# Performance work log

Hardware: AMD Instinct MI355X
Metric: run time of the kernel (lower is better)

The kernel has to match this reference:

```python
import jax, jax.numpy as jnp
import numpy as np

B, T, D = 8, 2048, 1024
DK, DV = 1024, 1024


def setup_inputs() -> dict:
    key = jax.random.key(0)
    ks = jax.random.split(key, 11)
    s = 0.02
    return {
        "query": jax.random.normal(ks[0], (B, T, D), jnp.float32),
        "keys": jax.random.normal(ks[1], (B, T, D), jnp.float32),
        "values": jax.random.normal(ks[2], (B, T, D), jnp.float32),
        "Wq": jax.random.normal(ks[3], (D, DK), jnp.float32) * s,
        "bq": jnp.zeros((DK,), jnp.float32),
        "Wk": jax.random.normal(ks[4], (D, DK), jnp.float32) * s,
        "bk": jnp.zeros((DK,), jnp.float32),
        "Wv": jax.random.normal(ks[5], (D, DV), jnp.float32) * s,
        "bv": jnp.zeros((DV,), jnp.float32),
        "Wo": jax.random.normal(ks[6], (DV, D), jnp.float32) * s,
        "bo": jnp.zeros((D,), jnp.float32),
        "apply_mask": 1,
    }


def reference(query, keys, values, Wq, bq, Wk, bk, Wv, bv, Wo, bo, apply_mask):
    # input projections
    q = query @ Wq + bq   # [B, T, DK]
    k = keys @ Wk + bk    # [B, T, DK]
    v = values @ Wv + bv  # [B, T, DV]
    dk = jnp.asarray(DK, jnp.float32)
    # explicit full score matrix, as in the original (non-flash) module
    scores = jnp.einsum("btd,bsd->bts", q, k) / jnp.sqrt(dk)  # [B, T, T]
    if apply_mask:
        Tq = q.shape[1]
        causal = jnp.triu(jnp.ones((Tq, Tq), bool), 1)  # True above diagonal
        scores = jnp.where(causal[None, :, :], -jnp.inf, scores)
    weights = jax.nn.softmax(scores, axis=-1)
    context = jnp.einsum("bts,bsd->btd", weights, v)  # [B, T, DV]
    return context @ Wo + bo  # [B, T, D]
```

## Files before the change

### kernel.cpp

```cpp
#include <hip/hip_runtime.h>
#include <hip/hip_bf16.h>


typedef __attribute__((ext_vector_type(8))) short bf16x8;
typedef __attribute__((ext_vector_type(4))) float f32x4;

#define DEVI __device__ __forceinline__
#define VM_GATE(n) asm volatile("s_waitcnt vmcnt(" #n ")" ::: "memory")
#define LGKM0()    asm volatile("s_waitcnt lgkmcnt(0)" ::: "memory")

DEVI unsigned short f2bf(float f) {
  union { float f; unsigned u; } v; v.f = f;
  unsigned r = v.u + 0x7FFFu + ((v.u >> 16) & 1u);
  return (unsigned short)(r >> 16);
}

DEVI unsigned pkbf(float a, float b) {
  unsigned r;
  asm("v_cvt_pk_bf16_f32 %0, %1, %2" : "=v"(r) : "v"(a), "v"(b));
  return r;
}

DEVI void load_lds16(const void* g, void* l) {
  __builtin_amdgcn_global_load_lds(
      (const __attribute__((address_space(1))) unsigned int*)g,
      (__attribute__((address_space(3))) unsigned int*)l,
      16, 0, 0);
}

constexpr int BM = 256, BN = 256, BK = 64;

DEVI void stage_chunk(char* chunk, const unsigned short* src, long ldx,
                      int kbase, int tid) {
#pragma unroll
  for (int i = 0; i < 2; ++i) {
    int tloc = i * 512 + tid;
    int r = tloc >> 2, ps = tloc & 3;
    int q = (ps - (r >> 1)) & 3;
    load_lds16(src + (size_t)r * ldx + kbase + q * 8,
               chunk + (i * 512 + (tid & 0x1C0)) * 16);
  }
}

DEVI bf16x8 frag(const char* chunk, int r, int q0) {
  int sp = (q0 + (r >> 1)) & 3;
  return *(const bf16x8*)(chunk + r * 64 + sp * 16);
}

DEVI void a32_load(float4* fr, const float* src, long lda, int kbase, int tid) {
#pragma unroll
  for (int j = 0; j < 4; ++j) {
    int cell = j * 512 + tid;
    int r = cell >> 3, q = cell & 7;
    const float* p = src + (size_t)r * lda + kbase + q * 8;
    fr[2 * j]     = *(const float4*)p;
    fr[2 * j + 1] = *(const float4*)(p + 4);
  }
}
DEVI void a32_write(char* chunk0, char* chunk1, const float4* fr, int tid) {
#pragma unroll
  for (int j = 0; j < 4; ++j) {
    int cell = j * 512 + tid;
    int r = cell >> 3, q = cell & 7;
    int kh = q >> 2, qq = q & 3;
    int sp = (qq + (r >> 1)) & 3;
    uint4 u;
    u.x = pkbf(fr[2 * j].x,     fr[2 * j].y);
    u.y = pkbf(fr[2 * j].z,     fr[2 * j].w);
    u.z = pkbf(fr[2 * j + 1].x, fr[2 * j + 1].y);
    u.w = pkbf(fr[2 * j + 1].z, fr[2 * j + 1].w);
    *(uint4*)((kh ? chunk1 : chunk0) + r * 64 + sp * 16) = u;
  }
}

template<bool A_F32, bool OUT_F32, bool OUT_TRANS, bool DO_BIAS, bool DO_SCALE,
         bool DO_CSKIP, bool DO_KCLAMP>
__global__ __launch_bounds__(512, 2) void gemm_k(
    const void* __restrict__ Ap, long lda, long sAz,
    const unsigned short* __restrict__ Bt, long ldb, long sBz,
    void* __restrict__ Cp, long ldc, long sCz,
    const float* __restrict__ bias, float scale,
    const int* __restrict__ maskp, int Kdim)
{
  const int nx = gridDim.x, ny = gridDim.y;
  int bid = (blockIdx.z * ny + blockIdx.y) * nx + blockIdx.x;
  const int nwg = nx * ny * (int)gridDim.z;
  if ((nwg & 7) == 0) bid = (bid & 7) * (nwg >> 3) + (bid >> 3);
  const int bx = bid % nx;
  const int t1 = bid / nx;
  const int by = t1 % ny;
  const int z  = t1 / ny;

  const int n0 = bx * BN;
  const int m0 = by * BM;
  if constexpr (DO_CSKIP) {
    if (maskp[0] && n0 > m0 + (BM - 1)) return;
  }
  int Keff = Kdim;
  if constexpr (DO_KCLAMP) {
    if (maskp[0]) Keff = min(Kdim, m0 + BM);
  }

  __shared__ alignas(16) char LDSb[2][2][2][16384];

  const int tid  = threadIdx.x;
  const int lane = tid & 63;
  const int w    = tid >> 6;
  const int wr   = w >> 2, wc = w & 3;
  const int la   = lane & 15;
  const int q0   = lane >> 4;

  f32x4 acc[8][4];
  const f32x4 z4 = {0.f, 0.f, 0.f, 0.f};
#pragma unroll
  for (int mi = 0; mi < 8; ++mi)
#pragma unroll
    for (int ni = 0; ni < 4; ++ni) acc[mi][ni] = z4;

  const unsigned short* Ag0 = (const unsigned short*)Ap + (size_t)z * sAz + (size_t)m0 * lda;
  const float*          Af0 = (const float*)Ap + (size_t)z * sAz + (size_t)m0 * lda;
  const unsigned short* Bg0 = Bt + (size_t)z * sBz + (size_t)n0 * ldb;

  float4 fr[8];

  if constexpr (A_F32) {
    a32_load(fr, Af0, lda, 0, tid);
    stage_chunk((char*)LDSb[0][1][0], Bg0, ldb, 0,  tid);
    stage_chunk((char*)LDSb[0][1][1], Bg0, ldb, 32, tid);
    VM_GATE(4);
    a32_write((char*)LDSb[0][0][0], (char*)LDSb[0][0][1], fr, tid);
    LGKM0();
  } else {
    stage_chunk((char*)LDSb[0][0][0], Ag0, lda, 0,  tid);
    stage_chunk((char*)LDSb[0][1][0], Bg0, ldb, 0,  tid);
    stage_chunk((char*)LDSb[0][0][1], Ag0, lda, 32, tid);
    stage_chunk((char*)LDSb[0][1][1], Bg0, ldb, 32, tid);
  }

  const int nt = Keff / BK;
  for (int t = 0; t < nt; ++t) {
    const int buf = t & 1, nb = buf ^ 1;
    const bool pf = (t + 1 < nt);
    const int kb = (t + 1) * BK;
    const char* Ak0 = LDSb[buf][0][0];
    const char* Bk0 = LDSb[buf][1][0];
    const char* Ak1 = LDSb[buf][0][1];
    const char* Bk1 = LDSb[buf][1][1];
    bf16x8 bfv0[4], bfv1[4], af[4];

    if constexpr (A_F32) { VM_GATE(2); } else { VM_GATE(4); }
    __builtin_amdgcn_s_barrier();
    __builtin_amdgcn_sched_barrier(0);
#pragma unroll
    for (int ni = 0; ni < 4; ++ni) bfv0[ni] = frag(Bk0, wc * 64 + ni * 16 + la, q0);
#pragma unroll
    for (int mi = 0; mi < 4; ++mi) af[mi] = frag(Ak0, wr * 128 + mi * 16 + la, q0);
    if (pf) {
      if constexpr (A_F32) a32_load(fr, Af0, lda, kb, tid);
      else stage_chunk((char*)LDSb[nb][0][0], Ag0, lda, kb, tid);
    }
    __builtin_amdgcn_s_setprio(1);
#pragma unroll
    for (int mi = 0; mi < 4; ++mi)
#pragma unroll
      for (int ni = 0; ni < 4; ++ni)
        acc[mi][ni] = __builtin_amdgcn_mfma_f32_16x16x32_bf16(af[mi], bfv0[ni], acc[mi][ni], 0, 0, 0);
    __builtin_amdgcn_s_setprio(0);

    __builtin_amdgcn_s_barrier();
    __builtin_amdgcn_sched_barrier(0);
#pragma unroll
    for (int mi = 0; mi < 4; ++mi) af[mi] = frag(Ak0, wr * 128 + 64 + mi * 16 + la, q0);
    if (pf) stage_chunk((char*)LDSb[nb][1][0], Bg0, ldb, kb, tid);
    __builtin_amdgcn_s_setprio(1);
#pragma unroll
    for (int mi = 0; mi < 4; ++mi)
#pragma unroll
      for (int ni = 0; ni < 4; ++ni)
        acc[4 + mi][ni] = __builtin_amdgcn_mfma_f32_16x16x32_bf16(af[mi], bfv0[ni], acc[4 + mi][ni], 0, 0, 0);
    __builtin_amdgcn_s_setprio(0);

    if constexpr (A_F32) {
      if (pf) { VM_GATE(2); } else { VM_GATE(0); }
    } else {
      if (pf) { VM_GATE(4); } else { VM_GATE(0); }
    }
    __builtin_amdgcn_s_barrier();
    __builtin_amdgcn_sched_barrier(0);
#pragma unroll
    for (int ni = 0; ni < 4; ++ni) bfv1[ni] = frag(Bk1, wc * 64 + ni * 16 + la, q0);
#pragma unroll
    for (int mi = 0; mi < 4; ++mi) af[mi] = frag(Ak1, wr * 128 + mi * 16 + la, q0);
    if (pf) {
      if constexpr (A_F32)
        a32_write((char*)LDSb[nb][0][0], (char*)LDSb[nb][0][1], fr, tid);
      else
        stage_chunk((char*)LDSb[nb][0][1], Ag0, lda, kb + 32, tid);
    }
    __builtin_amdgcn_s_setprio(1);
#pragma unroll
    for (int mi = 0; mi < 4; ++mi)
#pragma unroll
      for (int ni = 0; ni < 4; ++ni)
        acc[mi][ni] = __builtin_amdgcn_mfma_f32_16x16x32_bf16(af[mi], bfv1[ni], acc[mi][ni], 0, 0, 0);
    __builtin_amdgcn_s_setprio(0);

    __builtin_amdgcn_s_barrier();
    __builtin_amdgcn_sched_barrier(0);
#pragma unroll
    for (int mi = 0; mi < 4; ++mi) af[mi] = frag(Ak1, wr * 128 + 64 + mi * 16 + la, q0);
    if (pf) stage_chunk((char*)LDSb[nb][1][1], Bg0, ldb, kb + 32, tid);
    __builtin_amdgcn_s_setprio(1);
#pragma unroll
    for (int mi = 0; mi < 4; ++mi)
#pragma unroll
      for (int ni = 0; ni < 4; ++ni)
        acc[4 + mi][ni] = __builtin_amdgcn_mfma_f32_16x16x32_bf16(af[mi], bfv1[ni], acc[4 + mi][ni], 0, 0, 0);
    __builtin_amdgcn_s_setprio(0);
    if constexpr (A_F32) {
      if (pf) { LGKM0(); __builtin_amdgcn_sched_barrier(0); }
    }
  }

#pragma unroll
  for (int ni = 0; ni < 4; ++ni) {
    const int n = n0 + wc * 64 + ni * 16 + la;
    float bv = 0.f;
    if constexpr (DO_BIAS) bv = bias[n];
#pragma unroll
    for (int mi = 0; mi < 8; ++mi) {
      const int m = m0 + wr * 128 + mi * 16 + (q0 << 2);
      f32x4 c = acc[mi][ni];
      if constexpr (DO_SCALE) c = c * scale;
      if constexpr (DO_BIAS)  c = c + bv;
      if constexpr (OUT_TRANS) {
        unsigned short* C = (unsigned short*)Cp + (size_t)z * sCz + (size_t)n * ldc + m;
        ushort4 h;
        h.x = f2bf(c[0]); h.y = f2bf(c[1]); h.z = f2bf(c[2]); h.w = f2bf(c[3]);
        *(ushort4*)C = h;
      } else if constexpr (OUT_F32) {
        float* C = (float*)Cp + (size_t)z * sCz + (size_t)m * ldc + n;
#pragma unroll
        for (int j = 0; j < 4; ++j) C[(size_t)j * ldc] = c[j];
      } else {
        unsigned short* C = (unsigned short*)Cp + (size_t)z * sCz + (size_t)m * ldc + n;
#pragma unroll
        for (int j = 0; j < 4; ++j) C[(size_t)j * ldc] = f2bf(c[j]);
      }
    }
  }
}

__global__ __launch_bounds__(256) void wtrans_k(const float* __restrict__ W,
                                                unsigned short* __restrict__ Wt)
{
  __shared__ unsigned short L[64][80];
  const int n0 = blockIdx.x * 64, k0 = blockIdx.y * 64;
  const int tid = threadIdx.x;
#pragma unroll
  for (int p = 0; p < 4; ++p) {
    int idx = tid + p * 256;
    int r = idx >> 4, c4 = idx & 15;
    float4 v = *(const float4*)(W + (size_t)(k0 + r) * 1024 + n0 + c4 * 4);
    L[c4 * 4 + 0][r] = f2bf(v.x);
    L[c4 * 4 + 1][r] = f2bf(v.y);
    L[c4 * 4 + 2][r] = f2bf(v.z);
    L[c4 * 4 + 3][r] = f2bf(v.w);
  }
  __syncthreads();
#pragma unroll
  for (int p = 0; p < 2; ++p) {
    int idx = tid + p * 256;
    int n = idx >> 3, c8 = idx & 7;
    int4 v = *(const int4*)(&L[n][c8 * 8]);
    *(int4*)(Wt + (size_t)(n0 + n) * 1024 + k0 + c8 * 8) = v;
  }
}

__global__ __launch_bounds__(256) void softmax_k(float* __restrict__ S,
                                                 const int* __restrict__ maskp)
{
  const int row = blockIdx.x;
  const int t = row & 2047;
  const int msk = maskp[0];
  const int lim  = msk ? (t + 1) : 2048;
  const int wlim = msk ? ((t & ~255) + 256) : 2048;
  float* Srow = S + (size_t)row * 2048;
  const int tid = threadIdx.x;
  const int cbase = tid * 8;

  float v[8];
  if (cbase < lim) {
    float4 a = *(const float4*)(Srow + cbase);
    float4 b = *(const float4*)(Srow + cbase + 4);
    v[0] = a.x; v[1] = a.y; v[2] = a.z; v[3] = a.w;
    v[4] = b.x; v[5] = b.y; v[6] = b.z; v[7] = b.w;
#pragma unroll
    for (int j = 0; j < 8; ++j)
      if (cbase + j >= lim) v[j] = -__builtin_inff();
  } else {
#pragma unroll
    for (int j = 0; j < 8; ++j) v[j] = -__builtin_inff();
  }

  float mx = v[0];
#pragma unroll
  for (int j = 1; j < 8; ++j) mx = fmaxf(mx, v[j]);
#pragma unroll
  for (int off = 32; off; off >>= 1) mx = fmaxf(mx, __shfl_xor(mx, off, 64));

  __shared__ float redm[4], reds[4];
  const int wid = tid >> 6;
  if ((tid & 63) == 0) redm[wid] = mx;
  __syncthreads();
  mx = fmaxf(fmaxf(redm[0], redm[1]), fmaxf(redm[2], redm[3]));

  float e[8], s = 0.f;
#pragma unroll
  for (int j = 0; j < 8; ++j) { e[j] = __expf(v[j] - mx); s += e[j]; }
#pragma unroll
  for (int off = 32; off; off >>= 1) s += __shfl_xor(s, off, 64);
  if ((tid & 63) == 0) reds[wid] = s;
  __syncthreads();
  s = reds[0] + reds[1] + reds[2] + reds[3];
  const float inv = 1.0f / s;

  if (cbase < wlim) {
    unsigned short* Prow = (unsigned short*)Srow;
    unsigned pk[4];
#pragma unroll
    for (int q = 0; q < 4; ++q)
      pk[q] = (unsigned)f2bf(e[2 * q] * inv) | ((unsigned)f2bf(e[2 * q + 1] * inv) << 16);
    int4 o; o.x = (int)pk[0]; o.y = (int)pk[1]; o.z = (int)pk[2]; o.w = (int)pk[3];
    *(int4*)(Prow + (size_t)cbase) = o;
  }
}

extern "C" void kernel_launch(void* const* d_in, const int* in_sizes, int n_in,
                              void* d_out, int out_size, void* d_ws, size_t ws_size,
                              hipStream_t stream)
{
  const float* query  = (const float*)d_in[0];
  const float* keys   = (const float*)d_in[1];
  const float* values = (const float*)d_in[2];
  const float* Wq = (const float*)d_in[3];
  const float* bq = (const float*)d_in[4];
  const float* Wk = (const float*)d_in[5];
  const float* bk = (const float*)d_in[6];
  const float* Wv = (const float*)d_in[7];
  const float* bv = (const float*)d_in[8];
  const float* Wo = (const float*)d_in[9];
  const float* bo = (const float*)d_in[10];
  const int* maskp = (const int*)d_in[11];
  float* out = (float*)d_out;

  char* ws = (char*)d_ws;
  const size_t MB = 1ull << 20;
  unsigned short* wt_q = (unsigned short*)(ws + 0 * MB);
  unsigned short* wt_k = (unsigned short*)(ws + 2 * MB);
  unsigned short* wt_v = (unsigned short*)(ws + 4 * MB);
  unsigned short* wt_o = (unsigned short*)(ws + 6 * MB);
  unsigned short* Qb   = (unsigned short*)(ws + 8 * MB);
  unsigned short* Kb   = (unsigned short*)(ws + 40 * MB);
  unsigned short* Vt   = (unsigned short*)(ws + 72 * MB);
  float*          S    = (float*)(ws + 104 * MB);
  unsigned short* ctx  = Qb;

  const dim3 blk(512);
  const long sXT = 2048l * 1024;

  wtrans_k<<<dim3(16, 16), dim3(256), 0, stream>>>(Wq, wt_q);
  wtrans_k<<<dim3(16, 16), dim3(256), 0, stream>>>(Wk, wt_k);
  wtrans_k<<<dim3(16, 16), dim3(256), 0, stream>>>(Wv, wt_v);
  wtrans_k<<<dim3(16, 16), dim3(256), 0, stream>>>(Wo, wt_o);

  gemm_k<true, false, false, true, false, false, false><<<dim3(4, 8, 8), blk, 0, stream>>>(
      query, 1024, sXT, wt_q, 1024, 0, Qb, 1024, sXT, bq, 1.f, nullptr, 1024);
  gemm_k<true, false, false, true, false, false, false><<<dim3(4, 8, 8), blk, 0, stream>>>(
      keys, 1024, sXT, wt_k, 1024, 0, Kb, 1024, sXT, bk, 1.f, nullptr, 1024);
  gemm_k<true, false, true, true, false, false, false><<<dim3(4, 8, 8), blk, 0, stream>>>(
      values, 1024, sXT, wt_v, 1024, 0, Vt, 2048, 1024l * 2048, bv, 1.f, nullptr, 1024);

  gemm_k<false, true, false, false, true, true, false><<<dim3(8, 8, 8), blk, 0, stream>>>(
      Qb, 1024, sXT, Kb, 1024, sXT, S, 2048, 2048l * 2048, nullptr, 0.03125f, maskp, 1024);

  softmax_k<<<dim3(16384), dim3(256), 0, stream>>>(S, maskp);

  gemm_k<false, false, false, false, false, false, true><<<dim3(4, 8, 8), blk, 0, stream>>>(
      (unsigned short*)S, 4096, 2048l * 4096, Vt, 2048, 1024l * 2048,
      ctx, 1024, sXT, nullptr, 1.f, maskp, 2048);

  gemm_k<false, true, false, true, false, false, false><<<dim3(4, 8, 8), blk, 0, stream>>>(
      ctx, 1024, sXT, wt_o, 1024, 0, out, 1024, sXT, bo, 1.f, nullptr, 1024);
}
```

Baseline: 354.4 us.

## Restructure GEMM k-loop into two phases with deeper fp32 A prefetch; batch weight transposes

The GEMM main loop moves from four half-tile phases to two full phases per k-step. Each phase loads all eight A fragments and four B fragments and issues 32 MFMAs. For fp32 A inputs, the global load of the next-next tile is issued a full iteration ahead, with adjusted vmcnt gates, so load latency overlaps more compute. The four weight-transpose launches are merged into one launch over blockIdx.z. The trade-off is higher register pressure from eight live A fragments plus the in-flight fp32 prefetch registers, which could reduce occupancy or cause spills.

```diff
diff --git a/kernel.cpp b/kernel.cpp
--- a/kernel.cpp
+++ b/kernel.cpp
@@ -121,6 +121,7 @@
   const float*          Af0 = (const float*)Ap + (size_t)z * sAz + (size_t)m0 * lda;
   const unsigned short* Bg0 = Bt + (size_t)z * sBz + (size_t)n0 * ldb;
 
+  const int nt = Keff / BK;
   float4 fr[8];
 
   if constexpr (A_F32) {
@@ -129,6 +130,7 @@
     stage_chunk((char*)LDSb[0][1][1], Bg0, ldb, 32, tid);
     VM_GATE(4);
     a32_write((char*)LDSb[0][0][0], (char*)LDSb[0][0][1], fr, tid);
+    if (nt > 1) a32_load(fr, Af0, lda, BK, tid);
     LGKM0();
   } else {
     stage_chunk((char*)LDSb[0][0][0], Ag0, lda, 0,  tid);
@@ -137,7 +139,6 @@
     stage_chunk((char*)LDSb[0][1][1], Bg0, ldb, 32, tid);
   }
 
-  const int nt = Keff / BK;
   for (int t = 0; t < nt; ++t) {
     const int buf = t & 1, nb = buf ^ 1;
     const bool pf = (t + 1 < nt);
@@ -146,76 +147,57 @@
     const char* Bk0 = LDSb[buf][1][0];
     const char* Ak1 = LDSb[buf][0][1];
     const char* Bk1 = LDSb[buf][1][1];
-    bf16x8 bfv0[4], bfv1[4], af[4];
-
-    if constexpr (A_F32) { VM_GATE(2); } else { VM_GATE(4); }
+    bf16x8 bfv[4], af[8];
+
+    if constexpr (A_F32) {
+      if (pf) { VM_GATE(10); } else { VM_GATE(2); }
+    } else {
+      VM_GATE(4);
+    }
     __builtin_amdgcn_s_barrier();
     __builtin_amdgcn_sched_barrier(0);
 #pragma unroll
-    for (int ni = 0; ni < 4; ++ni) bfv0[ni] = frag(Bk0, wc * 64 + ni * 16 + la, q0);
-#pragma unroll
-    for (int mi = 0; mi < 4; ++mi) af[mi] = frag(Ak0, wr * 128 + mi * 16 + la, q0);
+    for (int ni = 0; ni < 4; ++ni) bfv[ni] = frag(Bk0, wc * 64 + ni * 16 + la, q0);
+#pragma unroll
+    for (int mi = 0; mi < 8; ++mi) af[mi] = frag(Ak0, wr * 128 + mi * 16 + la, q0);
     if (pf) {
-      if constexpr (A_F32) a32_load(fr, Af0, lda, kb, tid);
-      else stage_chunk((char*)LDSb[nb][0][0], Ag0, lda, kb, tid);
+      if constexpr (!A_F32) stage_chunk((char*)LDSb[nb][0][0], Ag0, lda, kb, tid);
+      stage_chunk((char*)LDSb[nb][1][0], Bg0, ldb, kb, tid);
     }
     __builtin_amdgcn_s_setprio(1);
 #pragma unroll
-    for (int mi = 0; mi < 4; ++mi)
+    for (int mi = 0; mi < 8; ++mi)
 #pragma unroll
       for (int ni = 0; ni < 4; ++ni)
-        acc[mi][ni] = __builtin_amdgcn_mfma_f32_16x16x32_bf16(af[mi], bfv0[ni], acc[mi][ni], 0, 0, 0);
+        acc[mi][ni] = __builtin_amdgcn_mfma_f32_16x16x32_bf16(af[mi], bfv[ni], acc[mi][ni], 0, 0, 0);
     __builtin_amdgcn_s_setprio(0);
 
+    if constexpr (A_F32) {
+      if (pf) { VM_GATE(10); } else { VM_GATE(0); }
+    } else {
+      if (pf) { VM_GATE(4); } else { VM_GATE(0); }
+    }
     __builtin_amdgcn_s_barrier();
     __builtin_amdgcn_sched_barrier(0);
 #pragma unroll
-    for (int mi = 0; mi < 4; ++mi) af[mi] = frag(Ak0, wr * 128 + 64 + mi * 16 + la, q0);
-    if (pf) stage_chunk((char*)LDSb[nb][1][0], Bg0, ldb, kb, tid);
+    for (int ni = 0; ni < 4; ++ni) bfv[ni] = frag(Bk1, wc * 64 + ni * 16 + la, q0);
+#pragma unroll
+    for (int mi = 0; mi < 8; ++mi) af[mi] = frag(Ak1, wr * 128 + mi * 16 + la, q0);
+    if (pf) {
+      if constexpr (!A_F32) stage_chunk((char*)LDSb[nb][0][1], Ag0, lda, kb + 32, tid);
+      stage_chunk((char*)LDSb[nb][1][1], Bg0, ldb, kb + 32, tid);
+      if constexpr (A_F32) {
+        VM_GATE(4);
+        a32_write((char*)LDSb[nb][0][0], (char*)LDSb[nb][0][1], fr, tid);
+        if (t + 2 < nt) a32_load(fr, Af0, lda, kb + BK, tid);
+      }
+    }
     __builtin_amdgcn_s_setprio(1);
 #pragma unroll
-    for (int mi = 0; mi < 4; ++mi)
+    for (int mi = 0; mi < 8; ++mi)
 #pragma unroll
       for (int ni = 0; ni < 4; ++ni)
-        acc[4 + mi][ni] = __builtin_amdgcn_mfma_f32_16x16x32_bf16(af[mi], bfv0[ni], acc[4 + mi][ni], 0, 0, 0);
-    __builtin_amdgcn_s_setprio(0);
-
-    if constexpr (A_F32) {
-      if (pf) { VM_GATE(2); } else { VM_GATE(0); }
-    } else {
-      if (pf) { VM_GATE(4); } else { VM_GATE(0); }
-    }
-    __builtin_amdgcn_s_barrier();
-    __builtin_amdgcn_sched_barrier(0);
-#pragma unroll
-    for (int ni = 0; ni < 4; ++ni) bfv1[ni] = frag(Bk1, wc * 64 + ni * 16 + la, q0);
-#pragma unroll
-    for (int mi = 0; mi < 4; ++mi) af[mi] = frag(Ak1, wr * 128 + mi * 16 + la, q0);
-    if (pf) {
-      if constexpr (A_F32)
-        a32_write((char*)LDSb[nb][0][0], (char*)LDSb[nb][0][1], fr, tid);
-      else
-        stage_chunk((char*)LDSb[nb][0][1], Ag0, lda, kb + 32, tid);
-    }
-    __builtin_amdgcn_s_setprio(1);
-#pragma unroll
-    for (int mi = 0; mi < 4; ++mi)
-#pragma unroll
-      for (int ni = 0; ni < 4; ++ni)
-        acc[mi][ni] = __builtin_amdgcn_mfma_f32_16x16x32_bf16(af[mi], bfv1[ni], acc[mi][ni], 0, 0, 0);
-    __builtin_amdgcn_s_setprio(0);
-
-    __builtin_amdgcn_s_barrier();
-    __builtin_amdgcn_sched_barrier(0);
-#pragma unroll
-    for (int mi = 0; mi < 4; ++mi) af[mi] = frag(Ak1, wr * 128 + 64 + mi * 16 + la, q0);
-    if (pf) stage_chunk((char*)LDSb[nb][1][1], Bg0, ldb, kb + 32, tid);
-    __builtin_amdgcn_s_setprio(1);
-#pragma unroll
-    for (int mi = 0; mi < 4; ++mi)
-#pragma unroll
-      for (int ni = 0; ni < 4; ++ni)
-        acc[4 + mi][ni] = __builtin_amdgcn_mfma_f32_16x16x32_bf16(af[mi], bfv1[ni], acc[4 + mi][ni], 0, 0, 0);
+        acc[mi][ni] = __builtin_amdgcn_mfma_f32_16x16x32_bf16(af[mi], bfv[ni], acc[mi][ni], 0, 0, 0);
     __builtin_amdgcn_s_setprio(0);
     if constexpr (A_F32) {
       if (pf) { LGKM0(); __builtin_amdgcn_sched_barrier(0); }
@@ -251,9 +233,16 @@
   }
 }
 
-__global__ __launch_bounds__(256) void wtrans_k(const float* __restrict__ W,
-                                                unsigned short* __restrict__ Wt)
+__global__ __launch_bounds__(256) void wtrans_k(
+    const float* __restrict__ W0, const float* __restrict__ W1,
+    const float* __restrict__ W2, const float* __restrict__ W3,
+    unsigned short* __restrict__ T0, unsigned short* __restrict__ T1,
+    unsigned short* __restrict__ T2, unsigned short* __restrict__ T3)
 {
+  const float* W = blockIdx.z == 0 ? W0 : blockIdx.z == 1 ? W1
+                 : blockIdx.z == 2 ? W2 : W3;
+  unsigned short* Wt = blockIdx.z == 0 ? T0 : blockIdx.z == 1 ? T1
+                     : blockIdx.z == 2 ? T2 : T3;
   __shared__ unsigned short L[64][80];
   const int n0 = blockIdx.x * 64, k0 = blockIdx.y * 64;
   const int tid = threadIdx.x;
@@ -369,10 +358,8 @@
   const dim3 blk(512);
   const long sXT = 2048l * 1024;
 
-  wtrans_k<<<dim3(16, 16), dim3(256), 0, stream>>>(Wq, wt_q);
-  wtrans_k<<<dim3(16, 16), dim3(256), 0, stream>>>(Wk, wt_k);
-  wtrans_k<<<dim3(16, 16), dim3(256), 0, stream>>>(Wv, wt_v);
-  wtrans_k<<<dim3(16, 16), dim3(256), 0, stream>>>(Wo, wt_o);
+  wtrans_k<<<dim3(16, 16, 4), dim3(256), 0, stream>>>(
+      Wq, Wk, Wv, Wo, wt_q, wt_k, wt_v, wt_o);
 
   gemm_k<true, false, false, true, false, false, false><<<dim3(4, 8, 8), blk, 0, stream>>>(
       query, 1024, sXT, wt_q, 1024, 0, Qb, 1024, sXT, bq, 1.f, nullptr, 1024);
```

Result: faster. 326.9 us (-7.8%).
